# Kernel tuning notes

Measured on AMD Instinct MI355X. Metric: run time of the kernel, lower is better.

Reference implementation:

```python
import jax, jax.numpy as jnp
import numpy as np

N, E, B = 10000, 100000, 64
IN_DIM, EDGE_DIM = 16, 8
HID = [32, 64]
OUT_DIM = 128
BN_EPS = 1e-5


def setup_inputs() -> dict:
    key = jax.random.key(0)
    ks = iter(jax.random.split(key, 32))
    inp = {}
    inp["x"] = jax.random.normal(next(ks), (N, IN_DIM), dtype=jnp.float32)
    inp["edge_index"] = jax.random.randint(next(ks), (2, E), 0, N, dtype=jnp.int64)
    inp["edge_attr"] = jax.random.normal(next(ks), (E, EDGE_DIM), dtype=jnp.float32)
    inp["batch"] = jnp.sort(jax.random.randint(next(ks), (N,), 0, B, dtype=jnp.int64))
    inp["edge_batch"] = jax.random.randint(next(ks), (E,), 0, B, dtype=jnp.int64)
    pre = IN_DIM
    for i, hd in enumerate(HID):
        s = 1.0 / np.sqrt(EDGE_DIM)
        inp[f"w_nn{i}"] = jax.random.uniform(next(ks), (pre * hd, EDGE_DIM), jnp.float32, -s, s)
        inp[f"b_nn{i}"] = jax.random.uniform(next(ks), (pre * hd,), jnp.float32, -s, s)
        inp[f"root{i}"] = jax.random.normal(next(ks), (pre, hd), dtype=jnp.float32) / np.sqrt(pre)
        inp[f"bias{i}"] = jnp.zeros((hd,), dtype=jnp.float32)
        inp[f"gamma{i}"] = jnp.ones((hd,), dtype=jnp.float32)
        inp[f"beta{i}"] = jnp.zeros((hd,), dtype=jnp.float32)
        pre = hd
    s = 1.0 / np.sqrt(pre)
    inp["s_w"] = jax.random.uniform(next(ks), (OUT_DIM, pre), jnp.float32, -s, s)
    inp["s_b"] = jax.random.uniform(next(ks), (OUT_DIM,), jnp.float32, -s, s)
    inp["t_w"] = jax.random.uniform(next(ks), (OUT_DIM, pre), jnp.float32, -s, s)
    inp["t_b"] = jax.random.uniform(next(ks), (OUT_DIM,), jnp.float32, -s, s)
    return inp


def _nnconv(x, edge_index, edge_attr, w_nn, b_nn, root, bias, out_dim):
    src, dst = edge_index[0], edge_index[1]
    # per-edge weight matrices [E, in_dim, out_dim]
    W = (edge_attr @ w_nn.T + b_nn).reshape(edge_attr.shape[0], -1, out_dim)
    msg = jnp.einsum('ei,eio->eo', x[src], W)  # gather + per-edge matmul
    agg = jax.ops.segment_sum(msg, dst, num_segments=N)  # scatter-add
    return agg + x @ root + bias


def _bn(x, gamma, beta):
    mu = jnp.mean(x, axis=0)
    var = jnp.mean((x - mu) ** 2, axis=0)  # biased var (torch BN training)
    return gamma * (x - mu) * jax.lax.rsqrt(var + BN_EPS) + beta


def reference(x, edge_index, edge_attr, batch, edge_batch,
              w_nn0, b_nn0, root0, bias0, gamma0, beta0,
              w_nn1, b_nn1, root1, bias1, gamma1, beta1,
              s_w, s_b, t_w, t_b):
    x = jax.nn.relu(_bn(_nnconv(x, edge_index, edge_attr, w_nn0, b_nn0, root0, bias0, HID[0]), gamma0, beta0))
    x = jax.nn.relu(_bn(_nnconv(x, edge_index, edge_attr, w_nn1, b_nn1, root1, bias1, HID[1]), gamma1, beta1))
    s_x = jnp.clip(x @ s_w.T + s_b, -30.0, 30.0)
    t_x = x @ t_w.T + t_b
    f_x = jax.nn.sigmoid(-s_x) * jnp.tanh(t_x)  # 1/(1+exp(s)) == sigmoid(-s)
    return jax.ops.segment_sum(f_x, batch, num_segments=B)
```

## Files before the change

kernel.cpp:

```cpp
#include <hip/hip_runtime.h>
#include <hip/hip_fp16.h>
#include <math.h>

#define NN 10000
#define NE 100000
#define BN_EPS 1e-5f


__device__ __forceinline__ unsigned short f2bf(float f) {
  unsigned int u = __float_as_uint(f);
  u += 0x7FFF + ((u >> 16) & 1);
  return (unsigned short)(u >> 16);
}
__device__ __forceinline__ float bf2f(unsigned short h) {
  return __uint_as_float(((unsigned int)h) << 16);
}

__global__ __launch_bounds__(256) void k_prep(
    const float* __restrict__ w0, const float* __restrict__ b0,
    const float* __restrict__ root0,
    const float* __restrict__ w1, const float* __restrict__ b1,
    const float* __restrict__ root1,
    const float* __restrict__ s_w, const float* __restrict__ t_w,
    const int* __restrict__ ei, int2* __restrict__ ei2,
    float* __restrict__ wT0, float* __restrict__ wT1, float* __restrict__ wstT,
    float* __restrict__ st0, float* __restrict__ st1, float* __restrict__ out)
{
  int gid = blockIdx.x * 256 + threadIdx.x;
  int gsz = gridDim.x * 256;
  for (int e = gid; e < NE; e += gsz)
    ei2[e] = make_int2(ei[e], ei[NE + e]);
  for (int idx = gid; idx < 16 * 320; idx += gsz) {
    int i = idx / 320, c = idx - i * 320;
    float v;
    if (c < 256)      v = w0[(i * 32 + (c & 31)) * 8 + (c >> 5)];
    else if (c < 288) v = b0[i * 32 + (c - 256)];
    else              v = root0[i * 32 + (c - 288)];
    wT0[idx] = v;
  }
  for (int idx = gid; idx < 32 * 640; idx += gsz) {
    int i = idx / 640, c = idx - i * 640;
    float v;
    if (c < 512)      v = w1[(i * 64 + (c & 63)) * 8 + (c >> 6)];
    else if (c < 576) v = b1[i * 64 + (c - 512)];
    else              v = root1[i * 64 + (c - 576)];
    wT1[idx] = v;
  }
  for (int idx = gid; idx < 64 * 256; idx += gsz) {
    int i = idx >> 8, o = idx & 255;
    wstT[idx] = (o < 128) ? s_w[o * 64 + i] : t_w[(o - 128) * 64 + i];
  }
  for (int idx = gid; idx < 64 * 128; idx += gsz) out[idx] = 0.f;
  if (gid < 64)  st0[gid] = 0.f;
  if (gid < 128) st1[gid] = 0.f;
}

__global__ __launch_bounds__(320) void k_node0(
    const float* __restrict__ x, const float* __restrict__ wT0,
    const float* __restrict__ bias0,
    unsigned short* __restrict__ G0h, __half* __restrict__ h0h)
{
  int c = threadIdx.x;
  float wc[16];
#pragma unroll
  for (int i = 0; i < 16; ++i) wc[i] = wT0[i * 320 + c];
  float bi = (c >= 288) ? bias0[c - 288] : 0.f;

  int n0 = blockIdx.x * 10;
  for (int n = n0; n < n0 + 10; n += 2) {
    const float4* xa = (const float4*)(x + n * 16);
    float a0 = 0.f, a1 = 0.f;
#pragma unroll
    for (int q = 0; q < 4; ++q) {
      float4 v0 = xa[q], v1 = xa[q + 4];
      a0 = fmaf(v0.x, wc[4 * q + 0], a0); a1 = fmaf(v1.x, wc[4 * q + 0], a1);
      a0 = fmaf(v0.y, wc[4 * q + 1], a0); a1 = fmaf(v1.y, wc[4 * q + 1], a1);
      a0 = fmaf(v0.z, wc[4 * q + 2], a0); a1 = fmaf(v1.z, wc[4 * q + 2], a1);
      a0 = fmaf(v0.w, wc[4 * q + 3], a0); a1 = fmaf(v1.w, wc[4 * q + 3], a1);
    }
    if (c < 288) {
      G0h[n * 288 + c]       = f2bf(a0);
      G0h[(n + 1) * 288 + c] = f2bf(a1);
    } else {
      h0h[n * 32 + (c - 288)]       = __float2half(a0 + bi);
      h0h[(n + 1) * 32 + (c - 288)] = __float2half(a1 + bi);
    }
  }
}

__global__ __launch_bounds__(256) void k_edge0(
    const int2* __restrict__ ei2, const float* __restrict__ ea,
    const unsigned short* __restrict__ G0h, __half* __restrict__ h0h)
{
  int tid = threadIdx.x;
  int slot = tid >> 4;
  int oo = (tid & 15) * 2;
  int stride = gridDim.x * 16;
  for (int e = blockIdx.x * 16 + slot; e < NE; e += stride) {
    int2 sd = ei2[e];
    const unsigned short* gr = G0h + sd.x * 288;
    const float4* ep = (const float4*)(ea + (size_t)e * 8);
    float4 e0 = ep[0], e1 = ep[1];
    float m0 = bf2f(gr[256 + oo]), m1 = bf2f(gr[256 + oo + 1]);
#pragma unroll
    for (int k = 0; k < 8; ++k) {
      ushort2 g2 = *(const ushort2*)(gr + k * 32 + oo);
      float ek = (k < 4) ? ((k == 0) ? e0.x : (k == 1) ? e0.y : (k == 2) ? e0.z : e0.w)
                         : ((k == 4) ? e1.x : (k == 5) ? e1.y : (k == 6) ? e1.z : e1.w);
      m0 = fmaf(ek, bf2f(g2.x), m0);
      m1 = fmaf(ek, bf2f(g2.y), m1);
    }
    unsafeAtomicAdd((__half2*)(h0h + sd.y * 32 + oo), __floats2half2_rn(m0, m1));
  }
}

template <int C>
__global__ __launch_bounds__(256) void k_stats(
    const __half* __restrict__ hh, float* __restrict__ st)
{
  const int RPB = 256 / C;
  int tid = threadIdx.x;
  int col = tid % C, rg = tid / C;
  float s1 = 0.f, s2 = 0.f;
  int step = gridDim.x * RPB;
  for (int n = blockIdx.x * RPB + rg; n < NN; n += step) {
    float v = __half2float(hh[n * C + col]);
    s1 += v; s2 += v * v;
  }
  __shared__ float l1[256], l2[256];
  l1[tid] = s1; l2[tid] = s2;
  __syncthreads();
  if (tid < C) {
    for (int r = 1; r < RPB; ++r) { s1 += l1[r * C + tid]; s2 += l2[r * C + tid]; }
    unsafeAtomicAdd(&st[tid], s1);
    unsafeAtomicAdd(&st[C + tid], s2);
  }
}

__global__ __launch_bounds__(256) void k_x1(
    const __half* __restrict__ h0h, float* __restrict__ x1,
    const float* __restrict__ st0,
    const float* __restrict__ g0, const float* __restrict__ be0)
{
  __shared__ float sc[32], sh[32];
  int tid = threadIdx.x;
  if (tid < 32) {
    float mu  = st0[tid] * (1.0f / NN);
    float var = st0[32 + tid] * (1.0f / NN) - mu * mu;
    float s   = g0[tid] * rsqrtf(var + BN_EPS);
    sc[tid] = s;
    sh[tid] = be0[tid] - mu * s;
  }
  __syncthreads();
  const int NV = NN * 16;
  for (int i = blockIdx.x * 256 + tid; i < NV; i += gridDim.x * 256) {
    __half2 hv = ((const __half2*)h0h)[i];
    int c0 = (i * 2) & 31;
    float vx = fmaxf(fmaf(__half2float(hv.x), sc[c0],     sh[c0]),     0.f);
    float vy = fmaxf(fmaf(__half2float(hv.y), sc[c0 + 1], sh[c0 + 1]), 0.f);
    ((float2*)x1)[i] = make_float2(vx, vy);
  }
}

__global__ __launch_bounds__(320) void k_node1(
    const float* __restrict__ x1, const float* __restrict__ wT1,
    const float* __restrict__ bias1,
    unsigned short* __restrict__ G1h, __half* __restrict__ h1h)
{
  int t = threadIdx.x;
  float wa[32], wb[32];
#pragma unroll
  for (int i = 0; i < 32; ++i) {
    float2 w2 = *(const float2*)(wT1 + i * 640 + 2 * t);
    wa[i] = w2.x; wb[i] = w2.y;
  }
  float bia = 0.f, bib = 0.f;
  if (t >= 288) { bia = bias1[2 * (t - 288)]; bib = bias1[2 * (t - 288) + 1]; }

  int n0 = blockIdx.x * 10;
  for (int n = n0; n < n0 + 10; n += 2) {
    const float4* xa = (const float4*)(x1 + n * 32);
    float a00 = 0.f, a01 = 0.f, a10 = 0.f, a11 = 0.f;
#pragma unroll
    for (int q = 0; q < 8; ++q) {
      float4 v0 = xa[q], v1 = xa[q + 8];
      a00 = fmaf(v0.x, wa[4 * q + 0], a00); a01 = fmaf(v0.x, wb[4 * q + 0], a01);
      a00 = fmaf(v0.y, wa[4 * q + 1], a00); a01 = fmaf(v0.y, wb[4 * q + 1], a01);
      a00 = fmaf(v0.z, wa[4 * q + 2], a00); a01 = fmaf(v0.z, wb[4 * q + 2], a01);
      a00 = fmaf(v0.w, wa[4 * q + 3], a00); a01 = fmaf(v0.w, wb[4 * q + 3], a01);
      a10 = fmaf(v1.x, wa[4 * q + 0], a10); a11 = fmaf(v1.x, wb[4 * q + 0], a11);
      a10 = fmaf(v1.y, wa[4 * q + 1], a10); a11 = fmaf(v1.y, wb[4 * q + 1], a11);
      a10 = fmaf(v1.z, wa[4 * q + 2], a10); a11 = fmaf(v1.z, wb[4 * q + 2], a11);
      a10 = fmaf(v1.w, wa[4 * q + 3], a10); a11 = fmaf(v1.w, wb[4 * q + 3], a11);
    }
    if (t < 288) {
      *(ushort2*)(G1h + n * 576 + 2 * t)       = make_ushort2(f2bf(a00), f2bf(a01));
      *(ushort2*)(G1h + (n + 1) * 576 + 2 * t) = make_ushort2(f2bf(a10), f2bf(a11));
    } else {
      int o = 2 * (t - 288);
      *(__half2*)(h1h + n * 64 + o)       = __floats2half2_rn(a00 + bia, a01 + bib);
      *(__half2*)(h1h + (n + 1) * 64 + o) = __floats2half2_rn(a10 + bia, a11 + bib);
    }
  }
}

__global__ __launch_bounds__(256) void k_edge1(
    const int2* __restrict__ ei2, const float* __restrict__ ea,
    const unsigned short* __restrict__ G1h, __half* __restrict__ h1h)
{
  int tid = threadIdx.x;
  int slot = tid >> 5;
  int oo = (tid & 31) * 2;
  int stride = gridDim.x * 8;
  for (int e = blockIdx.x * 8 + slot; e < NE; e += stride) {
    int2 sd = ei2[e];
    const unsigned short* gr = G1h + sd.x * 576;
    const float4* ep = (const float4*)(ea + (size_t)e * 8);
    float4 e0 = ep[0], e1 = ep[1];
    float m0 = bf2f(gr[512 + oo]), m1 = bf2f(gr[512 + oo + 1]);
#pragma unroll
    for (int k = 0; k < 8; ++k) {
      ushort2 g2 = *(const ushort2*)(gr + k * 64 + oo);
      float ek = (k < 4) ? ((k == 0) ? e0.x : (k == 1) ? e0.y : (k == 2) ? e0.z : e0.w)
                         : ((k == 4) ? e1.x : (k == 5) ? e1.y : (k == 6) ? e1.z : e1.w);
      m0 = fmaf(ek, bf2f(g2.x), m0);
      m1 = fmaf(ek, bf2f(g2.y), m1);
    }
    unsafeAtomicAdd((__half2*)(h1h + sd.y * 64 + oo), __floats2half2_rn(m0, m1));
  }
}

__global__ __launch_bounds__(256) void k_x2(
    const __half* __restrict__ h1h, float* __restrict__ x2,
    const float* __restrict__ st1,
    const float* __restrict__ g1, const float* __restrict__ be1)
{
  __shared__ float sc[64], sh[64];
  int tid = threadIdx.x;
  if (tid < 64) {
    float mu  = st1[tid] * (1.0f / NN);
    float var = st1[64 + tid] * (1.0f / NN) - mu * mu;
    float s   = g1[tid] * rsqrtf(var + BN_EPS);
    sc[tid] = s;
    sh[tid] = be1[tid] - mu * s;
  }
  __syncthreads();
  const int NV = NN * 32;
  for (int i = blockIdx.x * 256 + tid; i < NV; i += gridDim.x * 256) {
    __half2 hv = ((const __half2*)h1h)[i];
    int c0 = (i * 2) & 63;
    float vx = fmaxf(fmaf(__half2float(hv.x), sc[c0],     sh[c0]),     0.f);
    float vy = fmaxf(fmaf(__half2float(hv.y), sc[c0 + 1], sh[c0 + 1]), 0.f);
    ((float2*)x2)[i] = make_float2(vx, vy);
  }
}

__global__ __launch_bounds__(256) void k_head(
    const float* __restrict__ x2, const float* __restrict__ wstT,
    const float* __restrict__ s_b, const float* __restrict__ t_b,
    const int* __restrict__ batch, float* __restrict__ out)
{
  int tid = threadIdx.x;
  int c = tid & 127, g = tid >> 7;
  int n0 = blockIdx.x * 20 + g * 10;
  int n1 = n0 + 10;
  if (n0 >= NN) return;
  if (n1 > NN) n1 = NN;

  float wsr[64], wtr[64];
#pragma unroll
  for (int k = 0; k < 64; ++k) {
    wsr[k] = wstT[k * 256 + c];
    wtr[k] = wstT[k * 256 + 128 + c];
  }
  float sb = s_b[c], tb = t_b[c];

  int bcur = batch[n0];
  float facc = 0.f;
  for (int n = n0; n < n1; ++n) {
    const float4* xr = (const float4*)(x2 + (size_t)n * 64);
    float as = 0.f, at = 0.f;
#pragma unroll
    for (int q = 0; q < 16; ++q) {
      float4 xv = xr[q];
      as = fmaf(xv.x, wsr[4 * q + 0], as); at = fmaf(xv.x, wtr[4 * q + 0], at);
      as = fmaf(xv.y, wsr[4 * q + 1], as); at = fmaf(xv.y, wtr[4 * q + 1], at);
      as = fmaf(xv.z, wsr[4 * q + 2], as); at = fmaf(xv.z, wtr[4 * q + 2], at);
      as = fmaf(xv.w, wsr[4 * q + 3], as); at = fmaf(xv.w, wtr[4 * q + 3], at);
    }
    float sv = fminf(30.f, fmaxf(-30.f, as + sb));
    float tv = at + tb;
    float f  = tanhf(tv) / (1.f + expf(sv));
    int b = batch[n];
    if (b != bcur) {
      unsafeAtomicAdd(&out[bcur * 128 + c], facc);
      bcur = b; facc = 0.f;
    }
    facc += f;
  }
  unsafeAtomicAdd(&out[bcur * 128 + c], facc);
}

extern "C" void kernel_launch(void* const* d_in, const int* in_sizes, int n_in,
                              void* d_out, int out_size, void* d_ws, size_t ws_size,
                              hipStream_t stream)
{
  const float* x     = (const float*)d_in[0];
  const int*   ei    = (const int*)d_in[1];
  const float* ea    = (const float*)d_in[2];
  const int*   batch = (const int*)d_in[3];
  const float* w0    = (const float*)d_in[5];
  const float* b0    = (const float*)d_in[6];
  const float* root0 = (const float*)d_in[7];
  const float* bias0 = (const float*)d_in[8];
  const float* g0    = (const float*)d_in[9];
  const float* be0   = (const float*)d_in[10];
  const float* w1    = (const float*)d_in[11];
  const float* b1    = (const float*)d_in[12];
  const float* root1 = (const float*)d_in[13];
  const float* bias1 = (const float*)d_in[14];
  const float* g1    = (const float*)d_in[15];
  const float* be1   = (const float*)d_in[16];
  const float* s_w   = (const float*)d_in[17];
  const float* s_b   = (const float*)d_in[18];
  const float* t_w   = (const float*)d_in[19];
  const float* t_b   = (const float*)d_in[20];
  float* out = (float*)d_out;

  float* ws   = (float*)d_ws;
  unsigned short* G0h = (unsigned short*)ws;  ws += 1440000;
  unsigned short* G1h = (unsigned short*)ws;  ws += 2880000;
  __half* h0h = (__half*)ws;  ws += 160000;
  __half* h1h = (__half*)ws;  ws += 320000;
  float* x1   = ws;  ws += 320000;
  float* x2   = ws;  ws += 640000;
  float* st0  = ws;  ws += 64;
  float* st1  = ws;  ws += 128;
  float* wstT = ws;  ws += 16384;
  float* wT0  = ws;  ws += 5120;
  float* wT1  = ws;  ws += 20480;
  int2* ei2   = (int2*)ws;

  hipLaunchKernelGGL(k_prep, dim3(64), dim3(256), 0, stream,
                     w0, b0, root0, w1, b1, root1, s_w, t_w, ei, ei2,
                     wT0, wT1, wstT, st0, st1, out);
  hipLaunchKernelGGL(k_node0, dim3(1000), dim3(320), 0, stream,
                     x, wT0, bias0, G0h, h0h);
  hipLaunchKernelGGL(k_edge0, dim3(2048), dim3(256), 0, stream,
                     ei2, ea, G0h, h0h);
  hipLaunchKernelGGL(k_stats<32>, dim3(256), dim3(256), 0, stream, h0h, st0);
  hipLaunchKernelGGL(k_x1, dim3(512), dim3(256), 0, stream, h0h, x1, st0, g0, be0);
  hipLaunchKernelGGL(k_node1, dim3(1000), dim3(320), 0, stream,
                     x1, wT1, bias1, G1h, h1h);
  hipLaunchKernelGGL(k_edge1, dim3(2048), dim3(256), 0, stream,
                     ei2, ea, G1h, h1h);
  hipLaunchKernelGGL(k_stats<64>, dim3(256), dim3(256), 0, stream, h1h, st1);
  hipLaunchKernelGGL(k_x2, dim3(512), dim3(256), 0, stream, h1h, x2, st1, g1, be1);
  hipLaunchKernelGGL(k_head, dim3(500), dim3(256), 0, stream,
                     x2, wstT, s_b, t_b, batch, out);
}
```

Measured before the change: 188.5 us.

## Fuse all stages into one persistent kernel with software grid barriers

Replaces the ten separate kernel launches with a single persistent kernel of 256 blocks. The stages are separated by an atomic-counter grid barrier, and the barrier counter is reset with a memset before each launch. This is meant to remove per-launch overhead and the idle gaps between small kernels. In exchange, each stage now runs on a fixed 256x320 grid with fewer resident waves, which may cut parallelism in the memory-bound edge scatter stages. Correctness also relies on all 256 blocks being co-resident.

```diff
diff --git a/kernel.cpp b/kernel.cpp
--- a/kernel.cpp
+++ b/kernel.cpp
@@ -5,6 +5,8 @@
 #define NN 10000
 #define NE 100000
 #define BN_EPS 1e-5f
+#define GRID 256
+#define BLK 320
 
 
 __device__ __forceinline__ unsigned short f2bf(float f) {
@@ -16,346 +18,339 @@
   return __uint_as_float(((unsigned int)h) << 16);
 }
 
-__global__ __launch_bounds__(256) void k_prep(
-    const float* __restrict__ w0, const float* __restrict__ b0,
-    const float* __restrict__ root0,
-    const float* __restrict__ w1, const float* __restrict__ b1,
-    const float* __restrict__ root1,
-    const float* __restrict__ s_w, const float* __restrict__ t_w,
-    const int* __restrict__ ei, int2* __restrict__ ei2,
-    float* __restrict__ wT0, float* __restrict__ wT1, float* __restrict__ wstT,
-    float* __restrict__ st0, float* __restrict__ st1, float* __restrict__ out)
+struct P {
+  const float *x; const int *ei; const float *ea; const int *batch;
+  const float *w0, *b0, *root0, *bias0, *g0, *be0;
+  const float *w1, *b1, *root1, *bias1, *g1, *be1;
+  const float *s_w, *s_b, *t_w, *t_b;
+  float *out;
+  unsigned short *G0h, *G1h; __half *h0h, *h1h;
+  float *x1, *x2, *st0, *st1, *wT0, *wT1, *wstT;
+  int2 *ei2; unsigned int *bar;
+};
+
+__device__ __forceinline__ void gbar(unsigned int* bar) {
+  __syncthreads();
+  if (threadIdx.x == 0) {
+    __threadfence();
+    unsigned t = atomicAdd(bar, 1u);
+    unsigned goal = (t / GRID + 1u) * GRID;
+    while (atomicAdd(bar, 0u) < goal) __builtin_amdgcn_s_sleep(4);
+    __threadfence();
+  }
+  __syncthreads();
+}
+
+__global__ __launch_bounds__(BLK, 2) void mega(P p)
 {
-  int gid = blockIdx.x * 256 + threadIdx.x;
-  int gsz = gridDim.x * 256;
+  const int tid = threadIdx.x;
+  const int blk = blockIdx.x;
+  const int gid = blk * BLK + tid;
+  const int gsz = GRID * BLK;
+  __shared__ float l1[BLK], l2[BLK];
+  __shared__ float sc[64], sh[64];
+
   for (int e = gid; e < NE; e += gsz)
-    ei2[e] = make_int2(ei[e], ei[NE + e]);
+    p.ei2[e] = make_int2(p.ei[e], p.ei[NE + e]);
   for (int idx = gid; idx < 16 * 320; idx += gsz) {
     int i = idx / 320, c = idx - i * 320;
     float v;
-    if (c < 256)      v = w0[(i * 32 + (c & 31)) * 8 + (c >> 5)];
-    else if (c < 288) v = b0[i * 32 + (c - 256)];
-    else              v = root0[i * 32 + (c - 288)];
-    wT0[idx] = v;
+    if (c < 256)      v = p.w0[(i * 32 + (c & 31)) * 8 + (c >> 5)];
+    else if (c < 288) v = p.b0[i * 32 + (c - 256)];
+    else              v = p.root0[i * 32 + (c - 288)];
+    p.wT0[idx] = v;
   }
   for (int idx = gid; idx < 32 * 640; idx += gsz) {
     int i = idx / 640, c = idx - i * 640;
     float v;
-    if (c < 512)      v = w1[(i * 64 + (c & 63)) * 8 + (c >> 6)];
-    else if (c < 576) v = b1[i * 64 + (c - 512)];
-    else              v = root1[i * 64 + (c - 576)];
-    wT1[idx] = v;
+    if (c < 512)      v = p.w1[(i * 64 + (c & 63)) * 8 + (c >> 6)];
+    else if (c < 576) v = p.b1[i * 64 + (c - 512)];
+    else              v = p.root1[i * 64 + (c - 576)];
+    p.wT1[idx] = v;
   }
   for (int idx = gid; idx < 64 * 256; idx += gsz) {
     int i = idx >> 8, o = idx & 255;
-    wstT[idx] = (o < 128) ? s_w[o * 64 + i] : t_w[(o - 128) * 64 + i];
-  }
-  for (int idx = gid; idx < 64 * 128; idx += gsz) out[idx] = 0.f;
-  if (gid < 64)  st0[gid] = 0.f;
-  if (gid < 128) st1[gid] = 0.f;
-}
-
-__global__ __launch_bounds__(320) void k_node0(
-    const float* __restrict__ x, const float* __restrict__ wT0,
-    const float* __restrict__ bias0,
-    unsigned short* __restrict__ G0h, __half* __restrict__ h0h)
-{
-  int c = threadIdx.x;
-  float wc[16];
-#pragma unroll
-  for (int i = 0; i < 16; ++i) wc[i] = wT0[i * 320 + c];
-  float bi = (c >= 288) ? bias0[c - 288] : 0.f;
-
-  int n0 = blockIdx.x * 10;
-  for (int n = n0; n < n0 + 10; n += 2) {
-    const float4* xa = (const float4*)(x + n * 16);
-    float a0 = 0.f, a1 = 0.f;
-#pragma unroll
-    for (int q = 0; q < 4; ++q) {
-      float4 v0 = xa[q], v1 = xa[q + 4];
-      a0 = fmaf(v0.x, wc[4 * q + 0], a0); a1 = fmaf(v1.x, wc[4 * q + 0], a1);
-      a0 = fmaf(v0.y, wc[4 * q + 1], a0); a1 = fmaf(v1.y, wc[4 * q + 1], a1);
-      a0 = fmaf(v0.z, wc[4 * q + 2], a0); a1 = fmaf(v1.z, wc[4 * q + 2], a1);
-      a0 = fmaf(v0.w, wc[4 * q + 3], a0); a1 = fmaf(v1.w, wc[4 * q + 3], a1);
-    }
-    if (c < 288) {
-      G0h[n * 288 + c]       = f2bf(a0);
-      G0h[(n + 1) * 288 + c] = f2bf(a1);
-    } else {
-      h0h[n * 32 + (c - 288)]       = __float2half(a0 + bi);
-      h0h[(n + 1) * 32 + (c - 288)] = __float2half(a1 + bi);
-    }
-  }
-}
-
-__global__ __launch_bounds__(256) void k_edge0(
-    const int2* __restrict__ ei2, const float* __restrict__ ea,
-    const unsigned short* __restrict__ G0h, __half* __restrict__ h0h)
-{
-  int tid = threadIdx.x;
-  int slot = tid >> 4;
-  int oo = (tid & 15) * 2;
-  int stride = gridDim.x * 16;
-  for (int e = blockIdx.x * 16 + slot; e < NE; e += stride) {
-    int2 sd = ei2[e];
-    const unsigned short* gr = G0h + sd.x * 288;
-    const float4* ep = (const float4*)(ea + (size_t)e * 8);
-    float4 e0 = ep[0], e1 = ep[1];
-    float m0 = bf2f(gr[256 + oo]), m1 = bf2f(gr[256 + oo + 1]);
-#pragma unroll
-    for (int k = 0; k < 8; ++k) {
-      ushort2 g2 = *(const ushort2*)(gr + k * 32 + oo);
-      float ek = (k < 4) ? ((k == 0) ? e0.x : (k == 1) ? e0.y : (k == 2) ? e0.z : e0.w)
-                         : ((k == 4) ? e1.x : (k == 5) ? e1.y : (k == 6) ? e1.z : e1.w);
-      m0 = fmaf(ek, bf2f(g2.x), m0);
-      m1 = fmaf(ek, bf2f(g2.y), m1);
-    }
-    unsafeAtomicAdd((__half2*)(h0h + sd.y * 32 + oo), __floats2half2_rn(m0, m1));
-  }
-}
-
-template <int C>
-__global__ __launch_bounds__(256) void k_stats(
-    const __half* __restrict__ hh, float* __restrict__ st)
-{
-  const int RPB = 256 / C;
-  int tid = threadIdx.x;
-  int col = tid % C, rg = tid / C;
-  float s1 = 0.f, s2 = 0.f;
-  int step = gridDim.x * RPB;
-  for (int n = blockIdx.x * RPB + rg; n < NN; n += step) {
-    float v = __half2float(hh[n * C + col]);
-    s1 += v; s2 += v * v;
-  }
-  __shared__ float l1[256], l2[256];
-  l1[tid] = s1; l2[tid] = s2;
-  __syncthreads();
-  if (tid < C) {
-    for (int r = 1; r < RPB; ++r) { s1 += l1[r * C + tid]; s2 += l2[r * C + tid]; }
-    unsafeAtomicAdd(&st[tid], s1);
-    unsafeAtomicAdd(&st[C + tid], s2);
-  }
-}
-
-__global__ __launch_bounds__(256) void k_x1(
-    const __half* __restrict__ h0h, float* __restrict__ x1,
-    const float* __restrict__ st0,
-    const float* __restrict__ g0, const float* __restrict__ be0)
-{
-  __shared__ float sc[32], sh[32];
-  int tid = threadIdx.x;
-  if (tid < 32) {
-    float mu  = st0[tid] * (1.0f / NN);
-    float var = st0[32 + tid] * (1.0f / NN) - mu * mu;
-    float s   = g0[tid] * rsqrtf(var + BN_EPS);
-    sc[tid] = s;
-    sh[tid] = be0[tid] - mu * s;
-  }
-  __syncthreads();
-  const int NV = NN * 16;
-  for (int i = blockIdx.x * 256 + tid; i < NV; i += gridDim.x * 256) {
-    __half2 hv = ((const __half2*)h0h)[i];
-    int c0 = (i * 2) & 31;
-    float vx = fmaxf(fmaf(__half2float(hv.x), sc[c0],     sh[c0]),     0.f);
-    float vy = fmaxf(fmaf(__half2float(hv.y), sc[c0 + 1], sh[c0 + 1]), 0.f);
-    ((float2*)x1)[i] = make_float2(vx, vy);
-  }
-}
-
-__global__ __launch_bounds__(320) void k_node1(
-    const float* __restrict__ x1, const float* __restrict__ wT1,
-    const float* __restrict__ bias1,
-    unsigned short* __restrict__ G1h, __half* __restrict__ h1h)
-{
-  int t = threadIdx.x;
-  float wa[32], wb[32];
-#pragma unroll
-  for (int i = 0; i < 32; ++i) {
-    float2 w2 = *(const float2*)(wT1 + i * 640 + 2 * t);
-    wa[i] = w2.x; wb[i] = w2.y;
-  }
-  float bia = 0.f, bib = 0.f;
-  if (t >= 288) { bia = bias1[2 * (t - 288)]; bib = bias1[2 * (t - 288) + 1]; }
-
-  int n0 = blockIdx.x * 10;
-  for (int n = n0; n < n0 + 10; n += 2) {
-    const float4* xa = (const float4*)(x1 + n * 32);
-    float a00 = 0.f, a01 = 0.f, a10 = 0.f, a11 = 0.f;
-#pragma unroll
-    for (int q = 0; q < 8; ++q) {
-      float4 v0 = xa[q], v1 = xa[q + 8];
-      a00 = fmaf(v0.x, wa[4 * q + 0], a00); a01 = fmaf(v0.x, wb[4 * q + 0], a01);
-      a00 = fmaf(v0.y, wa[4 * q + 1], a00); a01 = fmaf(v0.y, wb[4 * q + 1], a01);
-      a00 = fmaf(v0.z, wa[4 * q + 2], a00); a01 = fmaf(v0.z, wb[4 * q + 2], a01);
-      a00 = fmaf(v0.w, wa[4 * q + 3], a00); a01 = fmaf(v0.w, wb[4 * q + 3], a01);
-      a10 = fmaf(v1.x, wa[4 * q + 0], a10); a11 = fmaf(v1.x, wb[4 * q + 0], a11);
-      a10 = fmaf(v1.y, wa[4 * q + 1], a10); a11 = fmaf(v1.y, wb[4 * q + 1], a11);
-      a10 = fmaf(v1.z, wa[4 * q + 2], a10); a11 = fmaf(v1.z, wb[4 * q + 2], a11);
-      a10 = fmaf(v1.w, wa[4 * q + 3], a10); a11 = fmaf(v1.w, wb[4 * q + 3], a11);
-    }
-    if (t < 288) {
-      *(ushort2*)(G1h + n * 576 + 2 * t)       = make_ushort2(f2bf(a00), f2bf(a01));
-      *(ushort2*)(G1h + (n + 1) * 576 + 2 * t) = make_ushort2(f2bf(a10), f2bf(a11));
-    } else {
-      int o = 2 * (t - 288);
-      *(__half2*)(h1h + n * 64 + o)       = __floats2half2_rn(a00 + bia, a01 + bib);
-      *(__half2*)(h1h + (n + 1) * 64 + o) = __floats2half2_rn(a10 + bia, a11 + bib);
-    }
-  }
-}
-
-__global__ __launch_bounds__(256) void k_edge1(
-    const int2* __restrict__ ei2, const float* __restrict__ ea,
-    const unsigned short* __restrict__ G1h, __half* __restrict__ h1h)
-{
-  int tid = threadIdx.x;
-  int slot = tid >> 5;
-  int oo = (tid & 31) * 2;
-  int stride = gridDim.x * 8;
-  for (int e = blockIdx.x * 8 + slot; e < NE; e += stride) {
-    int2 sd = ei2[e];
-    const unsigned short* gr = G1h + sd.x * 576;
-    const float4* ep = (const float4*)(ea + (size_t)e * 8);
-    float4 e0 = ep[0], e1 = ep[1];
-    float m0 = bf2f(gr[512 + oo]), m1 = bf2f(gr[512 + oo + 1]);
-#pragma unroll
-    for (int k = 0; k < 8; ++k) {
-      ushort2 g2 = *(const ushort2*)(gr + k * 64 + oo);
-      float ek = (k < 4) ? ((k == 0) ? e0.x : (k == 1) ? e0.y : (k == 2) ? e0.z : e0.w)
-                         : ((k == 4) ? e1.x : (k == 5) ? e1.y : (k == 6) ? e1.z : e1.w);
-      m0 = fmaf(ek, bf2f(g2.x), m0);
-      m1 = fmaf(ek, bf2f(g2.y), m1);
-    }
-    unsafeAtomicAdd((__half2*)(h1h + sd.y * 64 + oo), __floats2half2_rn(m0, m1));
-  }
-}
-
-__global__ __launch_bounds__(256) void k_x2(
-    const __half* __restrict__ h1h, float* __restrict__ x2,
-    const float* __restrict__ st1,
-    const float* __restrict__ g1, const float* __restrict__ be1)
-{
-  __shared__ float sc[64], sh[64];
-  int tid = threadIdx.x;
-  if (tid < 64) {
-    float mu  = st1[tid] * (1.0f / NN);
-    float var = st1[64 + tid] * (1.0f / NN) - mu * mu;
-    float s   = g1[tid] * rsqrtf(var + BN_EPS);
-    sc[tid] = s;
-    sh[tid] = be1[tid] - mu * s;
-  }
-  __syncthreads();
-  const int NV = NN * 32;
-  for (int i = blockIdx.x * 256 + tid; i < NV; i += gridDim.x * 256) {
-    __half2 hv = ((const __half2*)h1h)[i];
-    int c0 = (i * 2) & 63;
-    float vx = fmaxf(fmaf(__half2float(hv.x), sc[c0],     sh[c0]),     0.f);
-    float vy = fmaxf(fmaf(__half2float(hv.y), sc[c0 + 1], sh[c0 + 1]), 0.f);
-    ((float2*)x2)[i] = make_float2(vx, vy);
-  }
-}
-
-__global__ __launch_bounds__(256) void k_head(
-    const float* __restrict__ x2, const float* __restrict__ wstT,
-    const float* __restrict__ s_b, const float* __restrict__ t_b,
-    const int* __restrict__ batch, float* __restrict__ out)
-{
-  int tid = threadIdx.x;
-  int c = tid & 127, g = tid >> 7;
-  int n0 = blockIdx.x * 20 + g * 10;
-  int n1 = n0 + 10;
-  if (n0 >= NN) return;
-  if (n1 > NN) n1 = NN;
-
-  float wsr[64], wtr[64];
-#pragma unroll
-  for (int k = 0; k < 64; ++k) {
-    wsr[k] = wstT[k * 256 + c];
-    wtr[k] = wstT[k * 256 + 128 + c];
-  }
-  float sb = s_b[c], tb = t_b[c];
-
-  int bcur = batch[n0];
-  float facc = 0.f;
-  for (int n = n0; n < n1; ++n) {
-    const float4* xr = (const float4*)(x2 + (size_t)n * 64);
-    float as = 0.f, at = 0.f;
-#pragma unroll
-    for (int q = 0; q < 16; ++q) {
-      float4 xv = xr[q];
-      as = fmaf(xv.x, wsr[4 * q + 0], as); at = fmaf(xv.x, wtr[4 * q + 0], at);
-      as = fmaf(xv.y, wsr[4 * q + 1], as); at = fmaf(xv.y, wtr[4 * q + 1], at);
-      as = fmaf(xv.z, wsr[4 * q + 2], as); at = fmaf(xv.z, wtr[4 * q + 2], at);
-      as = fmaf(xv.w, wsr[4 * q + 3], as); at = fmaf(xv.w, wtr[4 * q + 3], at);
-    }
-    float sv = fminf(30.f, fmaxf(-30.f, as + sb));
-    float tv = at + tb;
-    float f  = tanhf(tv) / (1.f + expf(sv));
-    int b = batch[n];
-    if (b != bcur) {
-      unsafeAtomicAdd(&out[bcur * 128 + c], facc);
-      bcur = b; facc = 0.f;
-    }
-    facc += f;
-  }
-  unsafeAtomicAdd(&out[bcur * 128 + c], facc);
+    p.wstT[idx] = (o < 128) ? p.s_w[o * 64 + i] : p.t_w[(o - 128) * 64 + i];
+  }
+  for (int idx = gid; idx < 64 * 128; idx += gsz) p.out[idx] = 0.f;
+  if (gid < 64)  p.st0[gid] = 0.f;
+  if (gid < 128) p.st1[gid] = 0.f;
+  gbar(p.bar);
+
+  {
+    int c = tid;
+    float wc[16];
+#pragma unroll
+    for (int i = 0; i < 16; ++i) wc[i] = p.wT0[i * 320 + c];
+    float bi = (c >= 288) ? p.bias0[c - 288] : 0.f;
+    for (int vb = blk; vb < 1000; vb += GRID) {
+      int n0 = vb * 10;
+      for (int n = n0; n < n0 + 10; n += 2) {
+        const float4* xa = (const float4*)(p.x + n * 16);
+        float a0 = 0.f, a1 = 0.f;
+#pragma unroll
+        for (int q = 0; q < 4; ++q) {
+          float4 v0 = xa[q], v1 = xa[q + 4];
+          a0 = fmaf(v0.x, wc[4*q+0], a0); a1 = fmaf(v1.x, wc[4*q+0], a1);
+          a0 = fmaf(v0.y, wc[4*q+1], a0); a1 = fmaf(v1.y, wc[4*q+1], a1);
+          a0 = fmaf(v0.z, wc[4*q+2], a0); a1 = fmaf(v1.z, wc[4*q+2], a1);
+          a0 = fmaf(v0.w, wc[4*q+3], a0); a1 = fmaf(v1.w, wc[4*q+3], a1);
+        }
+        if (c < 288) {
+          p.G0h[n * 288 + c]       = f2bf(a0);
+          p.G0h[(n + 1) * 288 + c] = f2bf(a1);
+        } else {
+          p.h0h[n * 32 + (c - 288)]       = __float2half(a0 + bi);
+          p.h0h[(n + 1) * 32 + (c - 288)] = __float2half(a1 + bi);
+        }
+      }
+    }
+  }
+  gbar(p.bar);
+
+  {
+    int slot = tid >> 4;
+    int oo = (tid & 15) * 2;
+    for (int e = blk * 20 + slot; e < NE; e += GRID * 20) {
+      int2 sd = p.ei2[e];
+      const unsigned short* gr = p.G0h + sd.x * 288;
+      const float4* ep = (const float4*)(p.ea + (size_t)e * 8);
+      float4 e0 = ep[0], e1 = ep[1];
+      float m0 = bf2f(gr[256 + oo]), m1 = bf2f(gr[256 + oo + 1]);
+#pragma unroll
+      for (int k = 0; k < 8; ++k) {
+        ushort2 g2 = *(const ushort2*)(gr + k * 32 + oo);
+        float ek = (k < 4) ? ((k==0)?e0.x:(k==1)?e0.y:(k==2)?e0.z:e0.w)
+                           : ((k==4)?e1.x:(k==5)?e1.y:(k==6)?e1.z:e1.w);
+        m0 = fmaf(ek, bf2f(g2.x), m0);
+        m1 = fmaf(ek, bf2f(g2.y), m1);
+      }
+      unsafeAtomicAdd((__half2*)(p.h0h + sd.y * 32 + oo), __floats2half2_rn(m0, m1));
+    }
+  }
+  gbar(p.bar);
+
+  {
+    const int C = 32, RPB = BLK / C;
+    int col = tid % C, rg = tid / C;
+    float s1 = 0.f, s2 = 0.f;
+    for (int n = blk * RPB + rg; n < NN; n += GRID * RPB) {
+      float v = __half2float(p.h0h[n * C + col]);
+      s1 += v; s2 += v * v;
+    }
+    l1[tid] = s1; l2[tid] = s2;
+    __syncthreads();
+    if (tid < C) {
+      for (int r = 1; r < RPB; ++r) { s1 += l1[r*C + tid]; s2 += l2[r*C + tid]; }
+      unsafeAtomicAdd(&p.st0[tid], s1);
+      unsafeAtomicAdd(&p.st0[C + tid], s2);
+    }
+  }
+  gbar(p.bar);
+
+  {
+    if (tid < 32) {
+      float mu  = p.st0[tid] * (1.0f / NN);
+      float var = p.st0[32 + tid] * (1.0f / NN) - mu * mu;
+      float s   = p.g0[tid] * rsqrtf(var + BN_EPS);
+      sc[tid] = s;
+      sh[tid] = p.be0[tid] - mu * s;
+    }
+    __syncthreads();
+    const int NV = NN * 16;
+    for (int i = gid; i < NV; i += gsz) {
+      __half2 hv = ((const __half2*)p.h0h)[i];
+      int c0 = (i * 2) & 31;
+      float vx = fmaxf(fmaf(__half2float(hv.x), sc[c0],     sh[c0]),     0.f);
+      float vy = fmaxf(fmaf(__half2float(hv.y), sc[c0 + 1], sh[c0 + 1]), 0.f);
+      ((float2*)p.x1)[i] = make_float2(vx, vy);
+    }
+  }
+  gbar(p.bar);
+
+  {
+    int t = tid;
+    float wa[32], wb[32];
+#pragma unroll
+    for (int i = 0; i < 32; ++i) {
+      float2 w2 = *(const float2*)(p.wT1 + i * 640 + 2 * t);
+      wa[i] = w2.x; wb[i] = w2.y;
+    }
+    float bia = 0.f, bib = 0.f;
+    if (t >= 288) { bia = p.bias1[2*(t-288)]; bib = p.bias1[2*(t-288)+1]; }
+    for (int vb = blk; vb < 1000; vb += GRID) {
+      int n0 = vb * 10;
+      for (int n = n0; n < n0 + 10; n += 2) {
+        const float4* xa = (const float4*)(p.x1 + n * 32);
+        float a00 = 0.f, a01 = 0.f, a10 = 0.f, a11 = 0.f;
+#pragma unroll
+        for (int q = 0; q < 8; ++q) {
+          float4 v0 = xa[q], v1 = xa[q + 8];
+          a00 = fmaf(v0.x, wa[4*q+0], a00); a01 = fmaf(v0.x, wb[4*q+0], a01);
+          a00 = fmaf(v0.y, wa[4*q+1], a00); a01 = fmaf(v0.y, wb[4*q+1], a01);
+          a00 = fmaf(v0.z, wa[4*q+2], a00); a01 = fmaf(v0.z, wb[4*q+2], a01);
+          a00 = fmaf(v0.w, wa[4*q+3], a00); a01 = fmaf(v0.w, wb[4*q+3], a01);
+          a10 = fmaf(v1.x, wa[4*q+0], a10); a11 = fmaf(v1.x, wb[4*q+0], a11);
+          a10 = fmaf(v1.y, wa[4*q+1], a10); a11 = fmaf(v1.y, wb[4*q+1], a11);
+          a10 = fmaf(v1.z, wa[4*q+2], a10); a11 = fmaf(v1.z, wb[4*q+2], a11);
+          a10 = fmaf(v1.w, wa[4*q+3], a10); a11 = fmaf(v1.w, wb[4*q+3], a11);
+        }
+        if (t < 288) {
+          *(ushort2*)(p.G1h + n * 576 + 2*t)       = make_ushort2(f2bf(a00), f2bf(a01));
+          *(ushort2*)(p.G1h + (n + 1) * 576 + 2*t) = make_ushort2(f2bf(a10), f2bf(a11));
+        } else {
+          int o = 2 * (t - 288);
+          *(__half2*)(p.h1h + n * 64 + o)       = __floats2half2_rn(a00 + bia, a01 + bib);
+          *(__half2*)(p.h1h + (n + 1) * 64 + o) = __floats2half2_rn(a10 + bia, a11 + bib);
+        }
+      }
+    }
+  }
+  gbar(p.bar);
+
+  {
+    int slot = tid >> 5;
+    int oo = (tid & 31) * 2;
+    for (int e = blk * 10 + slot; e < NE; e += GRID * 10) {
+      int2 sd = p.ei2[e];
+      const unsigned short* gr = p.G1h + sd.x * 576;
+      const float4* ep = (const float4*)(p.ea + (size_t)e * 8);
+      float4 e0 = ep[0], e1 = ep[1];
+      float m0 = bf2f(gr[512 + oo]), m1 = bf2f(gr[512 + oo + 1]);
+#pragma unroll
+      for (int k = 0; k < 8; ++k) {
+        ushort2 g2 = *(const ushort2*)(gr + k * 64 + oo);
+        float ek = (k < 4) ? ((k==0)?e0.x:(k==1)?e0.y:(k==2)?e0.z:e0.w)
+                           : ((k==4)?e1.x:(k==5)?e1.y:(k==6)?e1.z:e1.w);
+        m0 = fmaf(ek, bf2f(g2.x), m0);
+        m1 = fmaf(ek, bf2f(g2.y), m1);
+      }
+      unsafeAtomicAdd((__half2*)(p.h1h + sd.y * 64 + oo), __floats2half2_rn(m0, m1));
+    }
+  }
+  gbar(p.bar);
+
+  {
+    const int C = 64, RPB = BLK / C;
+    int col = tid % C, rg = tid / C;
+    float s1 = 0.f, s2 = 0.f;
+    for (int n = blk * RPB + rg; n < NN; n += GRID * RPB) {
+      float v = __half2float(p.h1h[n * C + col]);
+      s1 += v; s2 += v * v;
+    }
+    l1[tid] = s1; l2[tid] = s2;
+    __syncthreads();
+    if (tid < C) {
+      for (int r = 1; r < RPB; ++r) { s1 += l1[r*C + tid]; s2 += l2[r*C + tid]; }
+      unsafeAtomicAdd(&p.st1[tid], s1);
+      unsafeAtomicAdd(&p.st1[C + tid], s2);
+    }
+  }
+  gbar(p.bar);
+
+  {
+    if (tid < 64) {
+      float mu  = p.st1[tid] * (1.0f / NN);
+      float var = p.st1[64 + tid] * (1.0f / NN) - mu * mu;
+      float s   = p.g1[tid] * rsqrtf(var + BN_EPS);
+      sc[tid] = s;
+      sh[tid] = p.be1[tid] - mu * s;
+    }
+    __syncthreads();
+    const int NV = NN * 32;
+    for (int i = gid; i < NV; i += gsz) {
+      __half2 hv = ((const __half2*)p.h1h)[i];
+      int c0 = (i * 2) & 63;
+      float vx = fmaxf(fmaf(__half2float(hv.x), sc[c0],     sh[c0]),     0.f);
+      float vy = fmaxf(fmaf(__half2float(hv.y), sc[c0 + 1], sh[c0 + 1]), 0.f);
+      ((float2*)p.x2)[i] = make_float2(vx, vy);
+    }
+  }
+  gbar(p.bar);
+
+  if (tid < 256) {
+    int c = tid & 127, g = tid >> 7;
+    float wsr[64], wtr[64];
+#pragma unroll
+    for (int k = 0; k < 64; ++k) {
+      wsr[k] = p.wstT[k * 256 + c];
+      wtr[k] = p.wstT[k * 256 + 128 + c];
+    }
+    float sb = p.s_b[c], tb = p.t_b[c];
+    for (int vb = blk; vb < 500; vb += GRID) {
+      int n0 = vb * 20 + g * 10;
+      int n1 = n0 + 10; if (n1 > NN) n1 = NN;
+      if (n0 >= NN) continue;
+      int bcur = p.batch[n0];
+      float facc = 0.f;
+      for (int n = n0; n < n1; ++n) {
+        const float4* xr = (const float4*)(p.x2 + (size_t)n * 64);
+        float as = 0.f, at = 0.f;
+#pragma unroll
+        for (int q = 0; q < 16; ++q) {
+          float4 xv = xr[q];
+          as = fmaf(xv.x, wsr[4*q+0], as); at = fmaf(xv.x, wtr[4*q+0], at);
+          as = fmaf(xv.y, wsr[4*q+1], as); at = fmaf(xv.y, wtr[4*q+1], at);
+          as = fmaf(xv.z, wsr[4*q+2], as); at = fmaf(xv.z, wtr[4*q+2], at);
+          as = fmaf(xv.w, wsr[4*q+3], as); at = fmaf(xv.w, wtr[4*q+3], at);
+        }
+        float sv = fminf(30.f, fmaxf(-30.f, as + sb));
+        float tv = at + tb;
+        float f  = tanhf(tv) / (1.f + expf(sv));
+        int b = p.batch[n];
+        if (b != bcur) {
+          unsafeAtomicAdd(&p.out[bcur * 128 + c], facc);
+          bcur = b; facc = 0.f;
+        }
+        facc += f;
+      }
+      unsafeAtomicAdd(&p.out[bcur * 128 + c], facc);
+    }
+  }
 }
 
 extern "C" void kernel_launch(void* const* d_in, const int* in_sizes, int n_in,
                               void* d_out, int out_size, void* d_ws, size_t ws_size,
                               hipStream_t stream)
 {
-  const float* x     = (const float*)d_in[0];
-  const int*   ei    = (const int*)d_in[1];
-  const float* ea    = (const float*)d_in[2];
-  const int*   batch = (const int*)d_in[3];
-  const float* w0    = (const float*)d_in[5];
-  const float* b0    = (const float*)d_in[6];
-  const float* root0 = (const float*)d_in[7];
-  const float* bias0 = (const float*)d_in[8];
-  const float* g0    = (const float*)d_in[9];
-  const float* be0   = (const float*)d_in[10];
-  const float* w1    = (const float*)d_in[11];
-  const float* b1    = (const float*)d_in[12];
-  const float* root1 = (const float*)d_in[13];
-  const float* bias1 = (const float*)d_in[14];
-  const float* g1    = (const float*)d_in[15];
-  const float* be1   = (const float*)d_in[16];
-  const float* s_w   = (const float*)d_in[17];
-  const float* s_b   = (const float*)d_in[18];
-  const float* t_w   = (const float*)d_in[19];
-  const float* t_b   = (const float*)d_in[20];
-  float* out = (float*)d_out;
-
-  float* ws   = (float*)d_ws;
-  unsigned short* G0h = (unsigned short*)ws;  ws += 1440000;
-  unsigned short* G1h = (unsigned short*)ws;  ws += 2880000;
-  __half* h0h = (__half*)ws;  ws += 160000;
-  __half* h1h = (__half*)ws;  ws += 320000;
-  float* x1   = ws;  ws += 320000;
-  float* x2   = ws;  ws += 640000;
-  float* st0  = ws;  ws += 64;
-  float* st1  = ws;  ws += 128;
-  float* wstT = ws;  ws += 16384;
-  float* wT0  = ws;  ws += 5120;
-  float* wT1  = ws;  ws += 20480;
-  int2* ei2   = (int2*)ws;
-
-  hipLaunchKernelGGL(k_prep, dim3(64), dim3(256), 0, stream,
-                     w0, b0, root0, w1, b1, root1, s_w, t_w, ei, ei2,
-                     wT0, wT1, wstT, st0, st1, out);
-  hipLaunchKernelGGL(k_node0, dim3(1000), dim3(320), 0, stream,
-                     x, wT0, bias0, G0h, h0h);
-  hipLaunchKernelGGL(k_edge0, dim3(2048), dim3(256), 0, stream,
-                     ei2, ea, G0h, h0h);
-  hipLaunchKernelGGL(k_stats<32>, dim3(256), dim3(256), 0, stream, h0h, st0);
-  hipLaunchKernelGGL(k_x1, dim3(512), dim3(256), 0, stream, h0h, x1, st0, g0, be0);
-  hipLaunchKernelGGL(k_node1, dim3(1000), dim3(320), 0, stream,
-                     x1, wT1, bias1, G1h, h1h);
-  hipLaunchKernelGGL(k_edge1, dim3(2048), dim3(256), 0, stream,
-                     ei2, ea, G1h, h1h);
-  hipLaunchKernelGGL(k_stats<64>, dim3(256), dim3(256), 0, stream, h1h, st1);
-  hipLaunchKernelGGL(k_x2, dim3(512), dim3(256), 0, stream, h1h, x2, st1, g1, be1);
-  hipLaunchKernelGGL(k_head, dim3(500), dim3(256), 0, stream,
-                     x2, wstT, s_b, t_b, batch, out);
-}
+  P prm;
+  prm.x     = (const float*)d_in[0];
+  prm.ei    = (const int*)d_in[1];
+  prm.ea    = (const float*)d_in[2];
+  prm.batch = (const int*)d_in[3];
+  prm.w0    = (const float*)d_in[5];
+  prm.b0    = (const float*)d_in[6];
+  prm.root0 = (const float*)d_in[7];
+  prm.bias0 = (const float*)d_in[8];
+  prm.g0    = (const float*)d_in[9];
+  prm.be0   = (const float*)d_in[10];
+  prm.w1    = (const float*)d_in[11];
+  prm.b1    = (const float*)d_in[12];
+  prm.root1 = (const float*)d_in[13];
+  prm.bias1 = (const float*)d_in[14];
+  prm.g1    = (const float*)d_in[15];
+  prm.be1   = (const float*)d_in[16];
+  prm.s_w   = (const float*)d_in[17];
+  prm.s_b   = (const float*)d_in[18];
+  prm.t_w   = (const float*)d_in[19];
+  prm.t_b   = (const float*)d_in[20];
+  prm.out   = (float*)d_out;
+
+  float* ws = (float*)d_ws;
+  prm.G0h = (unsigned short*)ws;  ws += 1440000;
+  prm.G1h = (unsigned short*)ws;  ws += 2880000;
+  prm.h0h = (__half*)ws;          ws += 160000;
+  prm.h1h = (__half*)ws;          ws += 320000;
+  prm.x1  = ws;                   ws += 320000;
+  prm.x2  = ws;                   ws += 640000;
+  prm.st0 = ws;                   ws += 64;
+  prm.st1 = ws;                   ws += 128;
+  prm.wstT= ws;                   ws += 16384;
+  prm.wT0 = ws;                   ws += 5120;
+  prm.wT1 = ws;                   ws += 20480;
+  prm.ei2 = (int2*)ws;            ws += NE * 2;
+  prm.bar = (unsigned int*)ws;    ws += 16;
+
+  hipMemsetAsync((void*)prm.bar, 0, 64, stream);
+  hipLaunchKernelGGL(mega, dim3(GRID), dim3(BLK), 0, stream, prm);
+}
```

Result: slower. 353.4 us (+87.4%).

## Fuse BatchNorm+ReLU apply into node1 and head kernels via shared memory

Applied to the files above, without the earlier changes.

Removes the standalone k_x1 and k_x2 kernels that materialized normalized activations in fp32 global buffers. Each consumer kernel now computes the BN scale/shift from the stats, normalizes its own tile of half-precision pre-activations into shared memory, and reads from there. This drops two launches and a full write+read of the x1/x2 intermediates, at the cost of redundant per-block scale computation and extra barriers.

```diff
diff --git a/kernel.cpp b/kernel.cpp
--- a/kernel.cpp
+++ b/kernel.cpp
@@ -137,37 +137,25 @@
   }
 }
 
-__global__ __launch_bounds__(256) void k_x1(
-    const __half* __restrict__ h0h, float* __restrict__ x1,
-    const float* __restrict__ st0,
-    const float* __restrict__ g0, const float* __restrict__ be0)
+__global__ __launch_bounds__(320) void k_node1(
+    const __half* __restrict__ h0h, const float* __restrict__ st0,
+    const float* __restrict__ g0, const float* __restrict__ be0,
+    const float* __restrict__ wT1, const float* __restrict__ bias1,
+    unsigned short* __restrict__ G1h, __half* __restrict__ h1h)
 {
   __shared__ float sc[32], sh[32];
-  int tid = threadIdx.x;
-  if (tid < 32) {
-    float mu  = st0[tid] * (1.0f / NN);
-    float var = st0[32 + tid] * (1.0f / NN) - mu * mu;
-    float s   = g0[tid] * rsqrtf(var + BN_EPS);
-    sc[tid] = s;
-    sh[tid] = be0[tid] - mu * s;
-  }
-  __syncthreads();
-  const int NV = NN * 16;
-  for (int i = blockIdx.x * 256 + tid; i < NV; i += gridDim.x * 256) {
-    __half2 hv = ((const __half2*)h0h)[i];
-    int c0 = (i * 2) & 31;
-    float vx = fmaxf(fmaf(__half2float(hv.x), sc[c0],     sh[c0]),     0.f);
-    float vy = fmaxf(fmaf(__half2float(hv.y), sc[c0 + 1], sh[c0 + 1]), 0.f);
-    ((float2*)x1)[i] = make_float2(vx, vy);
-  }
-}
-
-__global__ __launch_bounds__(320) void k_node1(
-    const float* __restrict__ x1, const float* __restrict__ wT1,
-    const float* __restrict__ bias1,
-    unsigned short* __restrict__ G1h, __half* __restrict__ h1h)
-{
+  __shared__ float xs[320];
   int t = threadIdx.x;
+  int n0 = blockIdx.x * 10;
+
+  if (t < 32) {
+    float mu  = st0[t] * (1.0f / NN);
+    float var = st0[32 + t] * (1.0f / NN) - mu * mu;
+    float s   = g0[t] * rsqrtf(var + BN_EPS);
+    sc[t] = s;
+    sh[t] = be0[t] - mu * s;
+  }
+
   float wa[32], wb[32];
 #pragma unroll
   for (int i = 0; i < 32; ++i) {
@@ -177,9 +165,16 @@
   float bia = 0.f, bib = 0.f;
   if (t >= 288) { bia = bias1[2 * (t - 288)]; bib = bias1[2 * (t - 288) + 1]; }
 
-  int n0 = blockIdx.x * 10;
+  __syncthreads();
+  {
+    int col = t & 31;
+    float hv = __half2float(h0h[(n0 + (t >> 5)) * 32 + col]);
+    xs[t] = fmaxf(fmaf(hv, sc[col], sh[col]), 0.f);
+  }
+  __syncthreads();
+
   for (int n = n0; n < n0 + 10; n += 2) {
-    const float4* xa = (const float4*)(x1 + n * 32);
+    const float4* xa = (const float4*)(xs + (n - n0) * 32);
     float a00 = 0.f, a01 = 0.f, a10 = 0.f, a11 = 0.f;
 #pragma unroll
     for (int q = 0; q < 8; ++q) {
@@ -230,13 +225,18 @@
   }
 }
 
-__global__ __launch_bounds__(256) void k_x2(
-    const __half* __restrict__ h1h, float* __restrict__ x2,
-    const float* __restrict__ st1,
-    const float* __restrict__ g1, const float* __restrict__ be1)
+__global__ __launch_bounds__(256) void k_head(
+    const __half* __restrict__ h1h, const float* __restrict__ st1,
+    const float* __restrict__ g1, const float* __restrict__ be1,
+    const float* __restrict__ wstT,
+    const float* __restrict__ s_b, const float* __restrict__ t_b,
+    const int* __restrict__ batch, float* __restrict__ out)
 {
   __shared__ float sc[64], sh[64];
+  __shared__ float xs[1280];
   int tid = threadIdx.x;
+  int nb = blockIdx.x * 20;
+
   if (tid < 64) {
     float mu  = st1[tid] * (1.0f / NN);
     float var = st1[64 + tid] * (1.0f / NN) - mu * mu;
@@ -244,29 +244,8 @@
     sc[tid] = s;
     sh[tid] = be1[tid] - mu * s;
   }
-  __syncthreads();
-  const int NV = NN * 32;
-  for (int i = blockIdx.x * 256 + tid; i < NV; i += gridDim.x * 256) {
-    __half2 hv = ((const __half2*)h1h)[i];
-    int c0 = (i * 2) & 63;
-    float vx = fmaxf(fmaf(__half2float(hv.x), sc[c0],     sh[c0]),     0.f);
-    float vy = fmaxf(fmaf(__half2float(hv.y), sc[c0 + 1], sh[c0 + 1]), 0.f);
-    ((float2*)x2)[i] = make_float2(vx, vy);
-  }
-}
-
-__global__ __launch_bounds__(256) void k_head(
-    const float* __restrict__ x2, const float* __restrict__ wstT,
-    const float* __restrict__ s_b, const float* __restrict__ t_b,
-    const int* __restrict__ batch, float* __restrict__ out)
-{
-  int tid = threadIdx.x;
+
   int c = tid & 127, g = tid >> 7;
-  int n0 = blockIdx.x * 20 + g * 10;
-  int n1 = n0 + 10;
-  if (n0 >= NN) return;
-  if (n1 > NN) n1 = NN;
-
   float wsr[64], wtr[64];
 #pragma unroll
   for (int k = 0; k < 64; ++k) {
@@ -275,10 +254,22 @@
   }
   float sb = s_b[c], tb = t_b[c];
 
+  __syncthreads();
+#pragma unroll
+  for (int r = 0; r < 5; ++r) {
+    int i = tid + r * 256;
+    int col = i & 63;
+    float hv = __half2float(h1h[(size_t)(nb + (i >> 6)) * 64 + col]);
+    xs[i] = fmaxf(fmaf(hv, sc[col], sh[col]), 0.f);
+  }
+  __syncthreads();
+
+  int n0 = nb + g * 10;
+  int n1 = n0 + 10;
   int bcur = batch[n0];
   float facc = 0.f;
   for (int n = n0; n < n1; ++n) {
-    const float4* xr = (const float4*)(x2 + (size_t)n * 64);
+    const float4* xr = (const float4*)(xs + (n - nb) * 64);
     float as = 0.f, at = 0.f;
 #pragma unroll
     for (int q = 0; q < 16; ++q) {
@@ -332,8 +323,6 @@
   unsigned short* G1h = (unsigned short*)ws;  ws += 2880000;
   __half* h0h = (__half*)ws;  ws += 160000;
   __half* h1h = (__half*)ws;  ws += 320000;
-  float* x1   = ws;  ws += 320000;
-  float* x2   = ws;  ws += 640000;
   float* st0  = ws;  ws += 64;
   float* st1  = ws;  ws += 128;
   float* wstT = ws;  ws += 16384;
@@ -349,13 +338,11 @@
   hipLaunchKernelGGL(k_edge0, dim3(2048), dim3(256), 0, stream,
                      ei2, ea, G0h, h0h);
   hipLaunchKernelGGL(k_stats<32>, dim3(256), dim3(256), 0, stream, h0h, st0);
-  hipLaunchKernelGGL(k_x1, dim3(512), dim3(256), 0, stream, h0h, x1, st0, g0, be0);
   hipLaunchKernelGGL(k_node1, dim3(1000), dim3(320), 0, stream,
-                     x1, wT1, bias1, G1h, h1h);
+                     h0h, st0, g0, be0, wT1, bias1, G1h, h1h);
   hipLaunchKernelGGL(k_edge1, dim3(2048), dim3(256), 0, stream,
                      ei2, ea, G1h, h1h);
   hipLaunchKernelGGL(k_stats<64>, dim3(256), dim3(256), 0, stream, h1h, st1);
-  hipLaunchKernelGGL(k_x2, dim3(512), dim3(256), 0, stream, h1h, x2, st1, g1, be1);
   hipLaunchKernelGGL(k_head, dim3(500), dim3(256), 0, stream,
-                     x2, wstT, s_b, t_b, batch, out);
-}
+                     h1h, st1, g1, be1, wstT, s_b, t_b, batch, out);
+}
```

New measurement: 173.6 us. 1.09x faster.
